# Kernel tuning notes

Measured on AMD Instinct MI355X. Metric: run time of the kernel, lower is better.

## Reference

```python
import jax, jax.numpy as jnp
import numpy as np

EPS = 0.05
MAX_ITER = 100


def setup_inputs() -> dict:
    key = jax.random.key(0)
    k1, k2, k3 = jax.random.split(key, 3)
    B, D, N = 16, 64, 1024
    x = jax.random.normal(k1, (B, D, N), dtype=jnp.float32)
    y = jax.random.normal(k2, (B, D, N), dtype=jnp.float32)
    C = jax.random.uniform(k3, (B, N, N), dtype=jnp.float32)
    return {"x": x, "y": y, "C": C}


def reference(x, y, C):
    # x: (B, D, N), y: (B, D, N) -- only last dim (number of points) is used.
    B = C.shape[0]
    N = x.shape[-1]
    cons = jnp.full((B, N, 1), 1.0 / N, dtype=jnp.float32)  # (B, N, 1)
    U = jnp.exp(-C / EPS)          # (B, N, N)
    V = jnp.swapaxes(U, 1, 2)      # U^T, (B, N, N)

    def body(carry, _):
        mu, _ = carry
        nu = cons / jnp.matmul(U, mu)   # (B, N, 1)
        mu_new = cons / jnp.matmul(V, nu)
        return (mu_new, nu), None

    (mu, nu), _ = jax.lax.scan(body, (cons, cons), None, length=MAX_ITER)
    # T = mu * U * nu^T, broadcast over rows/cols
    T = mu * U * jnp.swapaxes(nu, 1, 2)  # (B, N, N)
    return T
```

## Files before the change

kernel.cpp:

```cpp
#include <hip/hip_runtime.h>
#include <math.h>

#define B_    16
#define N_    1024
#define G_    16
#define NW    8
#define ITERS 100

#define MUDEN_OFF   8192
#define MUDEN_BYTES (4 * B_ * N_ * 4)
#define NUG_OFF     (MUDEN_OFF + MUDEN_BYTES)
#define ZERO_BYTES  NUG_OFF

__device__ __forceinline__ float fast_div(float num, float den) {
    float r = __builtin_amdgcn_rcpf(den);
    r = r * (2.0f - den * r);
    return num * r;
}

__device__ __forceinline__ float wave_sum64(float x) {
#define DPP_ADD(ctrl)                                                   \
    x += __int_as_float(__builtin_amdgcn_update_dpp(                    \
            0, __float_as_int(x), ctrl, 0xf, 0xf, false));
    DPP_ADD(0x111)
    DPP_ADD(0x112)
    DPP_ADD(0x114)
    DPP_ADD(0x118)
    DPP_ADD(0x142)
    DPP_ADD(0x143)
#undef DPP_ADD
    return __int_as_float(__builtin_amdgcn_readlane(__float_as_int(x), 63));
}

__global__ __launch_bounds__(512, 2)
void sinkhorn_kernel(const float* __restrict__ C, float* __restrict__ out,
                     float* __restrict__ mu_den, float* __restrict__ nug,
                     unsigned int* __restrict__ cnt)
{
    __shared__ float part[NW * 1024];
    __shared__ float mu_s[N_];

    const int tid = threadIdx.x;
    const int w   = tid >> 6;
    const int l   = tid & 63;
    const int bid = blockIdx.x;
    const int xx = bid & 7, ss = bid >> 3;
    const int b = xx + ((ss >> 4) << 3);
    const int g = ss & 15;
    const int row0 = 64 * g + 8 * w;
    const float cons = 1.0f / 1024.0f;

    float u[8][16];
    {
        const float* Cb = C + (size_t)b * N_ * N_ + (size_t)row0 * N_;
        #pragma unroll
        for (int rr = 0; rr < 8; ++rr)
            #pragma unroll
            for (int ch = 0; ch < 4; ++ch) {
                float4 cv = *(const float4*)(Cb + (size_t)rr * N_ + 4 * l + 256 * ch);
                u[rr][4*ch+0] = expf(-20.0f * cv.x);
                u[rr][4*ch+1] = expf(-20.0f * cv.y);
                u[rr][4*ch+2] = expf(-20.0f * cv.z);
                u[rr][4*ch+3] = expf(-20.0f * cv.w);
            }
    }

    mu_s[tid]       = cons;
    mu_s[tid + 512] = cons;
    __syncthreads();

    for (int it = 0; it < ITERS; ++it) {
        float a0 = 0.f, a1 = 0.f, a2 = 0.f, a3 = 0.f;
        float a4 = 0.f, a5 = 0.f, a6 = 0.f, a7 = 0.f;
        #pragma unroll
        for (int ch = 0; ch < 4; ++ch) {
            float4 mv = *(const float4*)&mu_s[4 * l + 256 * ch];
#define PHA(rr) a##rr += u[rr][4*ch+0]*mv.x + u[rr][4*ch+1]*mv.y \
                       + u[rr][4*ch+2]*mv.z + u[rr][4*ch+3]*mv.w;
            PHA(0) PHA(1) PHA(2) PHA(3) PHA(4) PHA(5) PHA(6) PHA(7)
#undef PHA
        }
        a0 = wave_sum64(a0); a1 = wave_sum64(a1);
        a2 = wave_sum64(a2); a3 = wave_sum64(a3);
        a4 = wave_sum64(a4); a5 = wave_sum64(a5);
        a6 = wave_sum64(a6); a7 = wave_sum64(a7);
        float nu0 = fast_div(cons, a0), nu1 = fast_div(cons, a1);
        float nu2 = fast_div(cons, a2), nu3 = fast_div(cons, a3);
        float nu4 = fast_div(cons, a4), nu5 = fast_div(cons, a5);
        float nu6 = fast_div(cons, a6), nu7 = fast_div(cons, a7);

        if (it == ITERS - 1 && l < 8) {
            float nv = (l == 0) ? nu0 : (l == 1) ? nu1 : (l == 2) ? nu2 :
                       (l == 3) ? nu3 : (l == 4) ? nu4 : (l == 5) ? nu5 :
                       (l == 6) ? nu6 : nu7;
            __hip_atomic_store(&nug[b * N_ + row0 + l], nv,
                               __ATOMIC_RELAXED, __HIP_MEMORY_SCOPE_AGENT);
        }

        #pragma unroll
        for (int ch = 0; ch < 4; ++ch) {
            float4 p;
#define PB(s) (u[0][4*ch+s]*nu0 + u[1][4*ch+s]*nu1 + u[2][4*ch+s]*nu2 + \
               u[3][4*ch+s]*nu3 + u[4][4*ch+s]*nu4 + u[5][4*ch+s]*nu5 + \
               u[6][4*ch+s]*nu6 + u[7][4*ch+s]*nu7)
            p.x = PB(0); p.y = PB(1); p.z = PB(2); p.w = PB(3);
#undef PB
            *(float4*)&part[w * 1024 + 4 * l + 256 * ch] = p;
        }
        __syncthreads();

        const int buf = it & 3;
        {
            float s0 = 0.f, s1 = 0.f;
            #pragma unroll
            for (int w2 = 0; w2 < NW; ++w2) {
                s0 += part[w2 * 1024 + tid];
                s1 += part[w2 * 1024 + tid + 512];
            }
            float* md = &mu_den[((size_t)buf * B_ + b) * N_];
            unsafeAtomicAdd(md + tid,       s0);
            unsafeAtomicAdd(md + tid + 512, s1);
        }

        __syncthreads();
        if (tid == 0) {
            unsigned int* c = &cnt[b * ITERS + it];
            __hip_atomic_fetch_add(c, 1u, __ATOMIC_RELAXED, __HIP_MEMORY_SCOPE_AGENT);
            while (__hip_atomic_load(c, __ATOMIC_RELAXED, __HIP_MEMORY_SCOPE_AGENT) < G_)
                __builtin_amdgcn_s_sleep(1);
        }
        __syncthreads();

        {
            const float* mdb = &mu_den[((size_t)buf * B_ + b) * N_];
            float den0 = __hip_atomic_load(mdb + tid,
                                           __ATOMIC_RELAXED, __HIP_MEMORY_SCOPE_AGENT);
            float den1 = __hip_atomic_load(mdb + tid + 512,
                                           __ATOMIC_RELAXED, __HIP_MEMORY_SCOPE_AGENT);
            mu_s[tid]       = fast_div(cons, den0);
            mu_s[tid + 512] = fast_div(cons, den1);
        }
        if (tid < 64)
            __hip_atomic_store(&mu_den[((size_t)((it + 2) & 3) * B_ + b) * N_ + 64 * g + tid],
                               0.0f, __ATOMIC_RELAXED, __HIP_MEMORY_SCOPE_AGENT);
        __syncthreads();
    }

    float mu_i[8];
    #pragma unroll
    for (int rr = 0; rr < 8; ++rr)
        mu_i[rr] = mu_s[row0 + rr];

    float* ob = out + (size_t)b * N_ * N_ + (size_t)row0 * N_;
    #pragma unroll
    for (int ch = 0; ch < 4; ++ch) {
        const int cbase = b * N_ + 4 * l + 256 * ch;
        float4 nuv;
        nuv.x = __hip_atomic_load(&nug[cbase + 0], __ATOMIC_RELAXED, __HIP_MEMORY_SCOPE_AGENT);
        nuv.y = __hip_atomic_load(&nug[cbase + 1], __ATOMIC_RELAXED, __HIP_MEMORY_SCOPE_AGENT);
        nuv.z = __hip_atomic_load(&nug[cbase + 2], __ATOMIC_RELAXED, __HIP_MEMORY_SCOPE_AGENT);
        nuv.w = __hip_atomic_load(&nug[cbase + 3], __ATOMIC_RELAXED, __HIP_MEMORY_SCOPE_AGENT);
        #pragma unroll
        for (int rr = 0; rr < 8; ++rr) {
            float4 t;
            t.x = mu_i[rr] * u[rr][4*ch+0] * nuv.x;
            t.y = mu_i[rr] * u[rr][4*ch+1] * nuv.y;
            t.z = mu_i[rr] * u[rr][4*ch+2] * nuv.z;
            t.w = mu_i[rr] * u[rr][4*ch+3] * nuv.w;
            *(float4*)(ob + (size_t)rr * N_ + 4 * l + 256 * ch) = t;
        }
    }
}

extern "C" void kernel_launch(void* const* d_in, const int* in_sizes, int n_in,
                              void* d_out, int out_size, void* d_ws, size_t ws_size,
                              hipStream_t stream) {
    const float* C = (const float*)d_in[2];
    float* out = (float*)d_out;

    unsigned char* ws = (unsigned char*)d_ws;
    unsigned int* cnt = (unsigned int*)ws;
    float* mu_den = (float*)(ws + MUDEN_OFF);
    float* nug    = (float*)(ws + NUG_OFF);

    hipMemsetAsync(ws, 0, ZERO_BYTES, stream);
    hipLaunchKernelGGL(sinkhorn_kernel, dim3(256), dim3(512), 0, stream,
                       C, out, mu_den, nug, cnt);
}
```

Before: 377.4 us.

## Split each batch across 32 blocks and use packed fp32 math

Doubles the grid to 512 persistent blocks, so each batch is split into 32 groups of 32 rows. Each wave now holds 4 rows of U instead of 8, and the launch bound allows 4 blocks per CU. The matrix-vector products are rewritten with 2-wide float vectors so the compiler can emit packed FMAs. The aim is more parallelism and fewer registers per thread, at the cost of twice as many full-width global atomic adds per iteration and a wider cross-block spin barrier (32 arrivals instead of 16).

```diff
diff --git a/kernel.cpp b/kernel.cpp
--- a/kernel.cpp
+++ b/kernel.cpp
@@ -3,9 +3,11 @@
 
 #define B_    16
 #define N_    1024
-#define G_    16
+#define G_    32
 #define NW    8
 #define ITERS 100
+
+typedef __attribute__((ext_vector_type(2))) float f32x2;
 
 #define MUDEN_OFF   8192
 #define MUDEN_BYTES (4 * B_ * N_ * 4)
@@ -32,7 +34,7 @@
     return __int_as_float(__builtin_amdgcn_readlane(__float_as_int(x), 63));
 }
 
-__global__ __launch_bounds__(512, 2)
+__global__ __launch_bounds__(512, 4)
 void sinkhorn_kernel(const float* __restrict__ C, float* __restrict__ out,
                      float* __restrict__ mu_den, float* __restrict__ nug,
                      unsigned int* __restrict__ cnt)
@@ -44,24 +46,21 @@
     const int w   = tid >> 6;
     const int l   = tid & 63;
     const int bid = blockIdx.x;
-    const int xx = bid & 7, ss = bid >> 3;
-    const int b = xx + ((ss >> 4) << 3);
-    const int g = ss & 15;
-    const int row0 = 64 * g + 8 * w;
+    const int b = 2 * (bid & 7) + (bid >> 8);
+    const int g = (bid >> 3) & 31;
+    const int row0 = 32 * g + 4 * w;
     const float cons = 1.0f / 1024.0f;
 
-    float u[8][16];
+    f32x2 u2[4][8];
     {
         const float* Cb = C + (size_t)b * N_ * N_ + (size_t)row0 * N_;
         #pragma unroll
-        for (int rr = 0; rr < 8; ++rr)
+        for (int rr = 0; rr < 4; ++rr)
             #pragma unroll
             for (int ch = 0; ch < 4; ++ch) {
                 float4 cv = *(const float4*)(Cb + (size_t)rr * N_ + 4 * l + 256 * ch);
-                u[rr][4*ch+0] = expf(-20.0f * cv.x);
-                u[rr][4*ch+1] = expf(-20.0f * cv.y);
-                u[rr][4*ch+2] = expf(-20.0f * cv.z);
-                u[rr][4*ch+3] = expf(-20.0f * cv.w);
+                u2[rr][2*ch]   = (f32x2){expf(-20.0f * cv.x), expf(-20.0f * cv.y)};
+                u2[rr][2*ch+1] = (f32x2){expf(-20.0f * cv.z), expf(-20.0f * cv.w)};
             }
     }
 
@@ -70,41 +69,46 @@
     __syncthreads();
 
     for (int it = 0; it < ITERS; ++it) {
-        float a0 = 0.f, a1 = 0.f, a2 = 0.f, a3 = 0.f;
-        float a4 = 0.f, a5 = 0.f, a6 = 0.f, a7 = 0.f;
+        f32x2 a20 = (f32x2){0.f, 0.f}, a21 = (f32x2){0.f, 0.f};
+        f32x2 a22 = (f32x2){0.f, 0.f}, a23 = (f32x2){0.f, 0.f};
         #pragma unroll
         for (int ch = 0; ch < 4; ++ch) {
             float4 mv = *(const float4*)&mu_s[4 * l + 256 * ch];
-#define PHA(rr) a##rr += u[rr][4*ch+0]*mv.x + u[rr][4*ch+1]*mv.y \
-                       + u[rr][4*ch+2]*mv.z + u[rr][4*ch+3]*mv.w;
-            PHA(0) PHA(1) PHA(2) PHA(3) PHA(4) PHA(5) PHA(6) PHA(7)
-#undef PHA
+            const f32x2 m01 = (f32x2){mv.x, mv.y};
+            const f32x2 m23 = (f32x2){mv.z, mv.w};
+            a20 += u2[0][2*ch] * m01;  a20 += u2[0][2*ch+1] * m23;
+            a21 += u2[1][2*ch] * m01;  a21 += u2[1][2*ch+1] * m23;
+            a22 += u2[2][2*ch] * m01;  a22 += u2[2][2*ch+1] * m23;
+            a23 += u2[3][2*ch] * m01;  a23 += u2[3][2*ch+1] * m23;
         }
-        a0 = wave_sum64(a0); a1 = wave_sum64(a1);
-        a2 = wave_sum64(a2); a3 = wave_sum64(a3);
-        a4 = wave_sum64(a4); a5 = wave_sum64(a5);
-        a6 = wave_sum64(a6); a7 = wave_sum64(a7);
+        float a0 = wave_sum64(a20.x + a20.y);
+        float a1 = wave_sum64(a21.x + a21.y);
+        float a2 = wave_sum64(a22.x + a22.y);
+        float a3 = wave_sum64(a23.x + a23.y);
         float nu0 = fast_div(cons, a0), nu1 = fast_div(cons, a1);
         float nu2 = fast_div(cons, a2), nu3 = fast_div(cons, a3);
-        float nu4 = fast_div(cons, a4), nu5 = fast_div(cons, a5);
-        float nu6 = fast_div(cons, a6), nu7 = fast_div(cons, a7);
 
-        if (it == ITERS - 1 && l < 8) {
-            float nv = (l == 0) ? nu0 : (l == 1) ? nu1 : (l == 2) ? nu2 :
-                       (l == 3) ? nu3 : (l == 4) ? nu4 : (l == 5) ? nu5 :
-                       (l == 6) ? nu6 : nu7;
+        if (it == ITERS - 1 && l < 4) {
+            float nv = (l == 0) ? nu0 : (l == 1) ? nu1 : (l == 2) ? nu2 : nu3;
             __hip_atomic_store(&nug[b * N_ + row0 + l], nv,
                                __ATOMIC_RELAXED, __HIP_MEMORY_SCOPE_AGENT);
         }
 
+        const f32x2 nr0 = (f32x2){nu0, nu0}, nr1 = (f32x2){nu1, nu1};
+        const f32x2 nr2 = (f32x2){nu2, nu2}, nr3 = (f32x2){nu3, nu3};
+
         #pragma unroll
         for (int ch = 0; ch < 4; ++ch) {
+            f32x2 pxy = u2[0][2*ch] * nr0;
+            pxy += u2[1][2*ch] * nr1;
+            pxy += u2[2][2*ch] * nr2;
+            pxy += u2[3][2*ch] * nr3;
+            f32x2 pzw = u2[0][2*ch+1] * nr0;
+            pzw += u2[1][2*ch+1] * nr1;
+            pzw += u2[2][2*ch+1] * nr2;
+            pzw += u2[3][2*ch+1] * nr3;
             float4 p;
-#define PB(s) (u[0][4*ch+s]*nu0 + u[1][4*ch+s]*nu1 + u[2][4*ch+s]*nu2 + \
-               u[3][4*ch+s]*nu3 + u[4][4*ch+s]*nu4 + u[5][4*ch+s]*nu5 + \
-               u[6][4*ch+s]*nu6 + u[7][4*ch+s]*nu7)
-            p.x = PB(0); p.y = PB(1); p.z = PB(2); p.w = PB(3);
-#undef PB
+            p.x = pxy.x; p.y = pxy.y; p.z = pzw.x; p.w = pzw.y;
             *(float4*)&part[w * 1024 + 4 * l + 256 * ch] = p;
         }
         __syncthreads();
@@ -140,15 +144,15 @@
             mu_s[tid]       = fast_div(cons, den0);
             mu_s[tid + 512] = fast_div(cons, den1);
         }
-        if (tid < 64)
-            __hip_atomic_store(&mu_den[((size_t)((it + 2) & 3) * B_ + b) * N_ + 64 * g + tid],
+        if (tid < 32)
+            __hip_atomic_store(&mu_den[((size_t)((it + 2) & 3) * B_ + b) * N_ + 32 * g + tid],
                                0.0f, __ATOMIC_RELAXED, __HIP_MEMORY_SCOPE_AGENT);
         __syncthreads();
     }
 
-    float mu_i[8];
+    float mu_i[4];
     #pragma unroll
-    for (int rr = 0; rr < 8; ++rr)
+    for (int rr = 0; rr < 4; ++rr)
         mu_i[rr] = mu_s[row0 + rr];
 
     float* ob = out + (size_t)b * N_ * N_ + (size_t)row0 * N_;
@@ -160,13 +164,15 @@
         nuv.y = __hip_atomic_load(&nug[cbase + 1], __ATOMIC_RELAXED, __HIP_MEMORY_SCOPE_AGENT);
         nuv.z = __hip_atomic_load(&nug[cbase + 2], __ATOMIC_RELAXED, __HIP_MEMORY_SCOPE_AGENT);
         nuv.w = __hip_atomic_load(&nug[cbase + 3], __ATOMIC_RELAXED, __HIP_MEMORY_SCOPE_AGENT);
+        const f32x2 nv01 = (f32x2){nuv.x, nuv.y};
+        const f32x2 nv23 = (f32x2){nuv.z, nuv.w};
         #pragma unroll
-        for (int rr = 0; rr < 8; ++rr) {
+        for (int rr = 0; rr < 4; ++rr) {
+            const f32x2 mu2v = (f32x2){mu_i[rr], mu_i[rr]};
+            f32x2 t01 = mu2v * u2[rr][2*ch]   * nv01;
+            f32x2 t23 = mu2v * u2[rr][2*ch+1] * nv23;
             float4 t;
-            t.x = mu_i[rr] * u[rr][4*ch+0] * nuv.x;
-            t.y = mu_i[rr] * u[rr][4*ch+1] * nuv.y;
-            t.z = mu_i[rr] * u[rr][4*ch+2] * nuv.z;
-            t.w = mu_i[rr] * u[rr][4*ch+3] * nuv.w;
+            t.x = t01.x; t.y = t01.y; t.z = t23.x; t.w = t23.y;
             *(float4*)(ob + (size_t)rr * N_ + 4 * l + 256 * ch) = t;
         }
     }
@@ -184,6 +190,6 @@
     float* nug    = (float*)(ws + NUG_OFF);
 
     hipMemsetAsync(ws, 0, ZERO_BYTES, stream);
-    hipLaunchKernelGGL(sinkhorn_kernel, dim3(256), dim3(512), 0, stream,
+    hipLaunchKernelGGL(sinkhorn_kernel, dim3(512), dim3(512), 0, stream,
                        C, out, mu_den, nug, cnt);
 }
```

New measurement: 545.3 us. 1.44x slower.
